# Kernel tuning notes

Measured on AMD Instinct MI355X. Metric: run time of the kernel, lower is better.

## Reference

```python
import jax, jax.numpy as jnp
from jax import lax
import numpy as np

BIN_THR = 0.5
ENDPOINT_THR = 8.0
K_WEIGHT = 60.0
THIN_ITERS = 8  # fixed-iteration Zhang-Suen thinning (stand-in for skimage.skeletonize)


def _bce_with_logits(x, y):
    # elementwise binary_cross_entropy_with_logits, reduction='none'
    return jnp.maximum(x, 0.0) - x * y + jnp.log1p(jnp.exp(-jnp.abs(x)))


def _center_zero_kernel(size):
    k = np.ones((1, 1, size, size), dtype=np.float32)
    k[0, 0, size // 2, size // 2] = 0.0
    return jnp.asarray(k)


def _conv2d(img, kernel, pad):
    # img: [N, 1, H, W], kernel: [1, 1, k, k]
    return lax.conv_general_dilated(img, kernel, (1, 1), [(pad, pad), (pad, pad)])


def _thin_substep(img, sub):
    # img: [N, H, W] of {0,1} float32; one Zhang-Suen sub-iteration (sub is a static int)
    N, H, W = img.shape
    p = jnp.pad(img, ((0, 0), (1, 1), (1, 1)))
    sh = lambda dy, dx: p[:, 1 + dy:1 + dy + H, 1 + dx:1 + dx + W]
    # clockwise neighbors p2..p9: N, NE, E, SE, S, SW, W, NW
    nb = [sh(-1, 0), sh(-1, 1), sh(0, 1), sh(1, 1), sh(1, 0), sh(1, -1), sh(0, -1), sh(-1, -1)]
    Bn = sum(nb)  # neighbor count
    trans = sum(((nb[i] < 0.5) & (nb[(i + 1) % 8] > 0.5)).astype(jnp.int32) for i in range(8))
    c1 = (Bn >= 2.0) & (Bn <= 6.0) & (trans == 1)
    p2, p4, p6, p8 = nb[0], nb[2], nb[4], nb[6]
    if sub == 0:
        c2 = (p2 * p4 * p6 == 0.0) & (p4 * p6 * p8 == 0.0)
    else:
        c2 = (p2 * p4 * p8 == 0.0) & (p2 * p6 * p8 == 0.0)
    delete = (img > 0.5) & c1 & c2
    return jnp.where(delete, 0.0, img)


def _skeletonize(img):
    # img: [N, H, W] binary float32
    def body(i, a):
        a = _thin_substep(a, 0)
        a = _thin_substep(a, 1)
        return a
    return lax.fori_loop(0, THIN_ITERS, body, img)


def setup_inputs() -> dict:
    key = jax.random.key(0)
    kx, ky = jax.random.split(key)
    x = jax.random.normal(kx, (16, 4, 512, 512), dtype=jnp.float32)
    y = jax.random.uniform(ky, (16, 4, 512, 512), dtype=jnp.float32)
    return {"x": x, "y": y}


def reference(x, y):
    Bsz, Np, H, W = x.shape
    loss_map = _bce_with_logits(x, y)  # [B, Np, H, W]
    # binarize: softmax over dim 0, threshold -> {0,1}; detached in original
    s = jax.nn.softmax(x, axis=0)
    A = lax.stop_gradient(jnp.where(s >= BIN_THR, 1.0, 0.0))
    # skeletonize each 2D slice
    skel = _skeletonize(A.reshape(Bsz * Np, H, W))  # [B*Np, H, W]
    # endpoint map: 3x3 ones-with-zero-center conv, threshold at 8
    ep_k = _center_zero_kernel(3)
    c_map = _conv2d(skel[:, None], ep_k, pad=1)  # [B*Np, 1, H, W]
    C = (c_map >= ENDPOINT_THR).astype(jnp.float32)
    # weight map: 9x9 ones-with-zero-center conv * K
    nb_k = _center_zero_kernel(9)
    Wmap = _conv2d(C.reshape(Bsz * Np, 1, H, W), nb_k, pad=4) * K_WEIGHT
    Wmap = Wmap.reshape(Bsz, Np, H, W)
    return jnp.mean(loss_map * Wmap)
```

## Files before the change

kernel.cpp:

```cpp
#include <hip/hip_runtime.h>
#include <cstdint>

#define HH 512
#define WW 512
#define NBATCH 16
#define NPRED 4
#define WPR 8
#define NELEM (NBATCH*NPRED*HH*WW)
#define HALO 21
#define OUTR 64
#define NRTOT (OUTR + 2*HALO)
#define LP (WPR+2)
#define NBLK 512
#define NTHR 256


static __device__ __forceinline__ void fadd(uint64_t a, uint64_t b, uint64_t ci,
                                            uint64_t& s, uint64_t& co) {
    uint64_t x = a ^ b;
    s  = x ^ ci;
    co = (a & b) | (ci & x);
}

static __device__ __forceinline__ void faddio(uint64_t& a, uint64_t b, uint64_t& c) {
    uint64_t x = a ^ b;
    uint64_t s = x ^ c;
    c = (a & b) | (c & x);
    a = s;
}

static __device__ __forceinline__ void sum8(const uint64_t q[8],
                                            uint64_t& b0, uint64_t& b1,
                                            uint64_t& b2, uint64_t& b3) {
    uint64_t s0,c0,s1,c1,s2,c2;
    fadd(q[0],q[1],q[2], s0,c0);
    fadd(q[3],q[4],q[5], s1,c1);
    s2 = q[6] ^ q[7]; c2 = q[6] & q[7];
    uint64_t ca; fadd(s0,s1,s2, b0, ca);
    uint64_t t, cb; fadd(c0,c1,c2, t, cb);
    b1 = t ^ ca; uint64_t cc = t & ca;
    b2 = cb ^ cc; b3 = cb & cc;
}

static __device__ __forceinline__ void acc74(uint64_t w[7], uint64_t b0, uint64_t b1,
                                             uint64_t b2, uint64_t b3) {
    uint64_t c;
    { uint64_t x = w[0] ^ b0; c = w[0] & b0; w[0] = x; }
    faddio(w[1], b1, c);
    faddio(w[2], b2, c);
    faddio(w[3], b3, c);
    { uint64_t x = w[4] ^ c; c = w[4] & c; w[4] = x; }
    { uint64_t x = w[5] ^ c; c = w[5] & c; w[5] = x; }
    w[6] ^= c;
}


__global__ void k_binarize(const float* __restrict__ x, uint64_t* __restrict__ pack) {
    int tid = blockIdx.x * blockDim.x + threadIdx.x;
    int w = tid & (WW-1);
    int h = (tid >> 9) & (HH-1);
    int p = tid >> 18;
    int lane = threadIdx.x & 63;
    float v[NBATCH], e[NBATCH];
    float m = -3.4e38f;
    int base = (p*HH + h)*WW + w;
    #pragma unroll
    for (int b = 0; b < NBATCH; ++b) {
        v[b] = x[(size_t)b*(NPRED*HH*WW) + base];
        m = fmaxf(m, v[b]);
    }
    float S = 0.f;
    #pragma unroll
    for (int b = 0; b < NBATCH; ++b) { e[b] = expf(v[b] - m); S += e[b]; }
    float hS = 0.5f * S;
    unsigned long long mymask = 0ULL;
    #pragma unroll
    for (int b = 0; b < NBATCH; ++b) {
        unsigned long long mk = __ballot(e[b] >= hS);
        if (lane == b) mymask = mk;
    }
    if (lane < NBATCH) {
        int slice = lane * NPRED + p;
        pack[((size_t)slice*HH + h)*WPR + (w >> 6)] = mymask;
    }
}

__global__ __launch_bounds__(NTHR) void k_thin_wmap(const uint64_t* __restrict__ pack,
                                                    const float* __restrict__ x,
                                                    const float* __restrict__ y,
                                                    double* __restrict__ partials) {
    __shared__ uint64_t A[(NRTOT+2)*LP];
    __shared__ uint64_t B[(NRTOT+2)*LP];
    __shared__ uint64_t Hs[4*72*WPR];
    __shared__ int chg[16];
    __shared__ int cflag;
    __shared__ double sdata[NTHR];

    const int s    = blockIdx.x >> 3;
    const int base = (blockIdx.x & 7) << 6;
    const int R0   = base - HALO;
    const int tid  = threadIdx.x;

    for (int i = tid; i < (NRTOT+2)*LP; i += NTHR) { A[i] = 0; B[i] = 0; }
    if (tid < 16) chg[tid] = 0;
    if (tid == 0) cflag = 0;
    __syncthreads();
    for (int i = tid; i < NRTOT*WPR; i += NTHR) {
        int lr = i >> 3, c = i & 7;
        int r = R0 + lr;
        if ((unsigned)r < (unsigned)HH)
            A[(lr+1)*LP + c + 1] = pack[((size_t)s*HH + r)*WPR + c];
    }
    __syncthreads();

    uint64_t* cur = A; uint64_t* nxt = B;
    int stable = 0;
    for (int step = 0; step < 16; ++step) {
        if (stable >= 2) break;
        bool mych = false;
        for (int i = tid; i < NRTOT*WPR; i += NTHR) {
            int lr = i >> 3, c = i & 7;
            int o = (lr+1)*LP + c + 1;
            uint64_t up = cur[o-LP-1], uc = cur[o-LP], un = cur[o-LP+1];
            uint64_t mp = cur[o-1],    mc = cur[o],    mn = cur[o+1];
            uint64_t dp = cur[o+LP-1], dc = cur[o+LP], dn = cur[o+LP+1];
            uint64_t p2 = uc;
            uint64_t p3 = (uc>>1)|(un<<63);
            uint64_t p4 = (mc>>1)|(mn<<63);
            uint64_t p5 = (dc>>1)|(dn<<63);
            uint64_t p6 = dc;
            uint64_t p7 = (dc<<1)|(dp>>63);
            uint64_t p8 = (mc<<1)|(mp>>63);
            uint64_t p9 = (uc<<1)|(up>>63);
            uint64_t qq[8] = {p2,p3,p4,p5,p6,p7,p8,p9};
            uint64_t n0,n1,n2,n3; sum8(qq,n0,n1,n2,n3);
            uint64_t condB = (n1|n2|n3) & ~(n3 | (n2&n1&n0));
            uint64_t tq[8];
            #pragma unroll
            for (int k = 0; k < 8; ++k) tq[k] = ~qq[k] & qq[(k+1)&7];
            uint64_t t0,t1,t2,t3; sum8(tq,t0,t1,t2,t3);
            uint64_t trans1 = t0 & ~(t1|t2|t3);
            uint64_t cond2 = (step & 1) ? (~(p2&p4&p8) & ~(p2&p6&p8))
                                        : (~(p2&p4&p6) & ~(p4&p6&p8));
            uint64_t nv = mc & ~(condB & trans1 & cond2);
            nxt[o] = nv;
            mych |= (nv != mc);
        }
        if (mych) chg[step] = 1;
        __syncthreads();
        stable = chg[step] ? 0 : stable + 1;
        uint64_t* t = cur; cur = nxt; nxt = t;
    }

    uint64_t* Cb = nxt;
    for (int i = tid; i < 72*WPR; i += NTHR) {
        int lr = (i >> 3) + 17, c = i & 7;
        int o = (lr+1)*LP + c + 1;
        uint64_t up = cur[o-LP-1], uc = cur[o-LP], un = cur[o-LP+1];
        uint64_t mp = cur[o-1],    mc = cur[o],    mn = cur[o+1];
        uint64_t dp = cur[o+LP-1], dc = cur[o+LP], dn = cur[o+LP+1];
        uint64_t p3 = (uc>>1)|(un<<63);
        uint64_t p4 = (mc>>1)|(mn<<63);
        uint64_t p5 = (dc>>1)|(dn<<63);
        uint64_t p7 = (dc<<1)|(dp>>63);
        uint64_t p8 = (mc<<1)|(mp>>63);
        uint64_t p9 = (uc<<1)|(up>>63);
        uint64_t cv = uc & p3 & p4 & p5 & dc & p7 & p8 & p9;
        Cb[o] = cv;
        if (cv) cflag = 1;
    }
    __syncthreads();

    if (!cflag) {
        if (tid == 0) partials[blockIdx.x] = 0.0;
        return;
    }

    for (int i = tid; i < 72*WPR; i += NTHR) {
        int hr = i >> 3, c = i & 7;
        int o = (hr+18)*LP + c + 1;
        uint64_t mp = Cb[o-1], mc = Cb[o], mn = Cb[o+1];
        uint64_t m[8];
        m[0] = (mc>>1)|(mn<<63); m[1] = (mc>>2)|(mn<<62);
        m[2] = (mc>>3)|(mn<<61); m[3] = (mc>>4)|(mn<<60);
        m[4] = (mc<<1)|(mp>>63); m[5] = (mc<<2)|(mp>>62);
        m[6] = (mc<<3)|(mp>>61); m[7] = (mc<<4)|(mp>>60);
        uint64_t b0,b1,b2,b3; sum8(m,b0,b1,b2,b3);
        uint64_t inc = mc;
        uint64_t s0 = b0 ^ inc; inc &= b0;
        uint64_t s1 = b1 ^ inc; inc &= b1;
        uint64_t s2 = b2 ^ inc; inc &= b2;
        uint64_t s3 = b3 ^ inc;
        Hs[0*576 + i] = s0; Hs[1*576 + i] = s1;
        Hs[2*576 + i] = s2; Hs[3*576 + i] = s3;
    }
    __syncthreads();

    double acc = 0.0;
    for (int i = tid; i < OUTR*WPR; i += NTHR) {
        int orr = i >> 3, c = i & 7;
        uint64_t w[7];
        int h0 = orr*WPR + c;
        w[0] = Hs[0*576 + h0]; w[1] = Hs[1*576 + h0];
        w[2] = Hs[2*576 + h0]; w[3] = Hs[3*576 + h0];
        w[4] = 0; w[5] = 0; w[6] = 0;
        #pragma unroll
        for (int d = 1; d < 9; ++d) {
            int hh = (orr+d)*WPR + c;
            acc74(w, Hs[0*576+hh], Hs[1*576+hh], Hs[2*576+hh], Hs[3*576+hh]);
        }
        uint64_t cb = Cb[(orr+HALO+1)*LP + c + 1];
        #pragma unroll
        for (int j = 0; j < 7; ++j) {
            uint64_t t = w[j];
            w[j] = t ^ cb;
            cb &= ~t;
        }
        uint64_t any = w[0]|w[1]|w[2]|w[3]|w[4]|w[5]|w[6];
        if (any) {
            size_t pix0 = ((size_t)s*HH + (base + orr))*WW + ((size_t)c << 6);
            uint64_t rem = any;
            while (rem) {
                int bit = __builtin_ctzll(rem);
                rem &= rem - 1;
                int wv = 0;
                #pragma unroll
                for (int j = 0; j < 7; ++j) wv |= (int)((w[j] >> bit) & 1ULL) << j;
                size_t idx = pix0 + bit;
                float lx = x[idx], ly = y[idx];
                float loss = fmaxf(lx, 0.f) - lx*ly + log1pf(expf(-fabsf(lx)));
                acc += (double)(loss * (60.0f * (float)wv));
            }
        }
    }
    sdata[tid] = acc;
    __syncthreads();
    for (int s2 = NTHR/2; s2 > 0; s2 >>= 1) {
        if (tid < s2) sdata[tid] += sdata[tid + s2];
        __syncthreads();
    }
    if (tid == 0) partials[blockIdx.x] = sdata[0];
}

__global__ void k_reduce(const double* __restrict__ partials, float* __restrict__ out,
                         int nparts) {
    __shared__ double sdata[256];
    double a = 0.0;
    for (int i = threadIdx.x; i < nparts; i += 256) a += partials[i];
    sdata[threadIdx.x] = a;
    __syncthreads();
    for (int s2 = 128; s2 > 0; s2 >>= 1) {
        if (threadIdx.x < s2) sdata[threadIdx.x] += sdata[threadIdx.x + s2];
        __syncthreads();
    }
    if (threadIdx.x == 0) out[0] = (float)(sdata[0] / (double)NELEM);
}


extern "C" void kernel_launch(void* const* d_in, const int* in_sizes, int n_in,
                              void* d_out, int out_size, void* d_ws, size_t ws_size,
                              hipStream_t stream) {
    const float* x = (const float*)d_in[0];
    const float* y = (const float*)d_in[1];
    char* ws = (char*)d_ws;
    uint64_t* packA    = (uint64_t*)(ws);
    double*   partials = (double*)  (ws + (2u<<20));

    k_binarize<<<4096, 256, 0, stream>>>(x, packA);
    k_thin_wmap<<<NBLK, NTHR, 0, stream>>>(packA, x, y, partials);
    k_reduce<<<1, 256, 0, stream>>>(partials, (float*)d_out, NBLK);
}
```

Baseline: 31.65 us.

## Vectorize binarize, halve thinning tiles, shrink halo per step, fuse final reduction

Binarize now loads float4 and uses a log-threshold test with fast exp/log, then transposes nibbles through shared memory to build packed words. The thinning kernel uses 32-row tiles over 1024 blocks and narrows the active row range each step as the valid halo shrinks, so rows that cannot affect the output are skipped. The histogram buffer reuses the ping-pong array, and the separate reduce kernel is replaced by a last-block-done atomic counter to save a launch. The price is more halo overhead per tile, a wider LDS row pitch, and a fast-math threshold that could flip borderline pixels.

```diff
diff --git a/kernel.cpp b/kernel.cpp
--- a/kernel.cpp
+++ b/kernel.cpp
@@ -8,11 +8,13 @@
 #define WPR 8
 #define NELEM (NBATCH*NPRED*HH*WW)
 #define HALO 21
-#define OUTR 64
+#define OUTR 32
 #define NRTOT (OUTR + 2*HALO)
-#define LP (WPR+2)
-#define NBLK 512
+#define LP 24
+#define NBLK 1024
 #define NTHR 256
+#define CROWS (OUTR + 8)
+#define HPL (CROWS*WPR)
 
 
 static __device__ __forceinline__ void fadd(uint64_t a, uint64_t b, uint64_t ci,
@@ -55,49 +57,66 @@
 }
 
 
-__global__ void k_binarize(const float* __restrict__ x, uint64_t* __restrict__ pack) {
-    int tid = blockIdx.x * blockDim.x + threadIdx.x;
-    int w = tid & (WW-1);
-    int h = (tid >> 9) & (HH-1);
-    int p = tid >> 18;
-    int lane = threadIdx.x & 63;
-    float v[NBATCH], e[NBATCH];
-    float m = -3.4e38f;
-    int base = (p*HH + h)*WW + w;
+__global__ __launch_bounds__(256) void k_binarize(const float* __restrict__ x,
+                                                  uint64_t* __restrict__ pack,
+                                                  unsigned int* __restrict__ cnt) {
+    if (blockIdx.x == 0 && threadIdx.x == 0) *cnt = 0u;
+    __shared__ uint64_t nibs[272];
+    const int t = blockIdx.x * 256 + threadIdx.x;
+    const float4* __restrict__ xv = reinterpret_cast<const float4*>(x);
+    float4 va[NBATCH];
+    #pragma unroll
+    for (int b = 0; b < NBATCH; ++b) va[b] = xv[(size_t)b * (NPRED*HH*WW/4) + t];
+    float4 mx = va[0];
+    #pragma unroll
+    for (int b = 1; b < NBATCH; ++b) {
+        mx.x = fmaxf(mx.x, va[b].x); mx.y = fmaxf(mx.y, va[b].y);
+        mx.z = fmaxf(mx.z, va[b].z); mx.w = fmaxf(mx.w, va[b].w);
+    }
+    float sx=0.f, sy=0.f, sz=0.f, sw=0.f;
     #pragma unroll
     for (int b = 0; b < NBATCH; ++b) {
-        v[b] = x[(size_t)b*(NPRED*HH*WW) + base];
-        m = fmaxf(m, v[b]);
-    }
-    float S = 0.f;
-    #pragma unroll
-    for (int b = 0; b < NBATCH; ++b) { e[b] = expf(v[b] - m); S += e[b]; }
-    float hS = 0.5f * S;
-    unsigned long long mymask = 0ULL;
+        sx += __expf(va[b].x - mx.x); sy += __expf(va[b].y - mx.y);
+        sz += __expf(va[b].z - mx.z); sw += __expf(va[b].w - mx.w);
+    }
+    const float tx = mx.x + __logf(0.5f*sx), ty = mx.y + __logf(0.5f*sy);
+    const float tz = mx.z + __logf(0.5f*sz), tw = mx.w + __logf(0.5f*sw);
+    uint64_t nib = 0;
     #pragma unroll
     for (int b = 0; b < NBATCH; ++b) {
-        unsigned long long mk = __ballot(e[b] >= hS);
-        if (lane == b) mymask = mk;
-    }
-    if (lane < NBATCH) {
-        int slice = lane * NPRED + p;
-        pack[((size_t)slice*HH + h)*WPR + (w >> 6)] = mymask;
-    }
+        unsigned n = (va[b].x >= tx ? 1u:0u) | (va[b].y >= ty ? 2u:0u)
+                   | (va[b].z >= tz ? 4u:0u) | (va[b].w >= tw ? 8u:0u);
+        nib |= (uint64_t)n << (4*b);
+    }
+    nibs[threadIdx.x + (threadIdx.x >> 4)] = nib;
+    __syncthreads();
+    const int wg = threadIdx.x >> 4, b = threadIdx.x & 15;
+    uint64_t word = 0;
+    #pragma unroll
+    for (int j = 0; j < 16; ++j)
+        word |= ((nibs[wg*17 + j] >> (4*b)) & 0xFULL) << (4*j);
+    const int wgg = blockIdx.x * 16 + wg;
+    const int wword = wgg & 7;
+    const int h = (wgg >> 3) & (HH-1);
+    const int p = wgg >> 12;
+    pack[((size_t)(b*NPRED + p)*HH + h)*WPR + wword] = word;
 }
 
 __global__ __launch_bounds__(NTHR) void k_thin_wmap(const uint64_t* __restrict__ pack,
                                                     const float* __restrict__ x,
                                                     const float* __restrict__ y,
-                                                    double* __restrict__ partials) {
+                                                    double* __restrict__ partials,
+                                                    unsigned int* __restrict__ cnt,
+                                                    float* __restrict__ out) {
     __shared__ uint64_t A[(NRTOT+2)*LP];
     __shared__ uint64_t B[(NRTOT+2)*LP];
-    __shared__ uint64_t Hs[4*72*WPR];
+    __shared__ double sdata[NTHR];
     __shared__ int chg[16];
     __shared__ int cflag;
-    __shared__ double sdata[NTHR];
-
-    const int s    = blockIdx.x >> 3;
-    const int base = (blockIdx.x & 7) << 6;
+    __shared__ int lastFlag;
+
+    const int s    = blockIdx.x >> 4;
+    const int base = (blockIdx.x & 15) << 5;
     const int R0   = base - HALO;
     const int tid  = threadIdx.x;
 
@@ -115,12 +134,14 @@
 
     uint64_t* cur = A; uint64_t* nxt = B;
     int stable = 0;
-    for (int step = 0; step < 16; ++step) {
-        if (stable >= 2) break;
+    for (int step = 0; step < 16 && stable < 2; ++step) {
+        const int lo = step + 1;
+        const int nw = (NRTOT - 2 - 2*step) * WPR;
         bool mych = false;
-        for (int i = tid; i < NRTOT*WPR; i += NTHR) {
-            int lr = i >> 3, c = i & 7;
-            int o = (lr+1)*LP + c + 1;
+        for (int i = tid; i < nw; i += NTHR) {
+            const int lr = (i >> 3) + lo;
+            const int c = i & 7;
+            const int o = (lr+1)*LP + c + 1;
             uint64_t up = cur[o-LP-1], uc = cur[o-LP], un = cur[o-LP+1];
             uint64_t mp = cur[o-1],    mc = cur[o],    mn = cur[o+1];
             uint64_t dp = cur[o+LP-1], dc = cur[o+LP], dn = cur[o+LP+1];
@@ -149,13 +170,14 @@
         if (mych) chg[step] = 1;
         __syncthreads();
         stable = chg[step] ? 0 : stable + 1;
-        uint64_t* t = cur; cur = nxt; nxt = t;
+        uint64_t* tmp = cur; cur = nxt; nxt = tmp;
     }
 
     uint64_t* Cb = nxt;
-    for (int i = tid; i < 72*WPR; i += NTHR) {
-        int lr = (i >> 3) + 17, c = i & 7;
-        int o = (lr+1)*LP + c + 1;
+    for (int i = tid; i < CROWS*WPR; i += NTHR) {
+        const int lr = (i >> 3) + (HALO - 4);
+        const int c = i & 7;
+        const int o = (lr+1)*LP + c + 1;
         uint64_t up = cur[o-LP-1], uc = cur[o-LP], un = cur[o-LP+1];
         uint64_t mp = cur[o-1],    mc = cur[o],    mn = cur[o+1];
         uint64_t dp = cur[o+LP-1], dc = cur[o+LP], dn = cur[o+LP+1];
@@ -171,89 +193,95 @@
     }
     __syncthreads();
 
-    if (!cflag) {
-        if (tid == 0) partials[blockIdx.x] = 0.0;
-        return;
-    }
-
-    for (int i = tid; i < 72*WPR; i += NTHR) {
-        int hr = i >> 3, c = i & 7;
-        int o = (hr+18)*LP + c + 1;
-        uint64_t mp = Cb[o-1], mc = Cb[o], mn = Cb[o+1];
-        uint64_t m[8];
-        m[0] = (mc>>1)|(mn<<63); m[1] = (mc>>2)|(mn<<62);
-        m[2] = (mc>>3)|(mn<<61); m[3] = (mc>>4)|(mn<<60);
-        m[4] = (mc<<1)|(mp>>63); m[5] = (mc<<2)|(mp>>62);
-        m[6] = (mc<<3)|(mp>>61); m[7] = (mc<<4)|(mp>>60);
-        uint64_t b0,b1,b2,b3; sum8(m,b0,b1,b2,b3);
-        uint64_t inc = mc;
-        uint64_t s0 = b0 ^ inc; inc &= b0;
-        uint64_t s1 = b1 ^ inc; inc &= b1;
-        uint64_t s2 = b2 ^ inc; inc &= b2;
-        uint64_t s3 = b3 ^ inc;
-        Hs[0*576 + i] = s0; Hs[1*576 + i] = s1;
-        Hs[2*576 + i] = s2; Hs[3*576 + i] = s3;
-    }
-    __syncthreads();
-
     double acc = 0.0;
-    for (int i = tid; i < OUTR*WPR; i += NTHR) {
-        int orr = i >> 3, c = i & 7;
-        uint64_t w[7];
-        int h0 = orr*WPR + c;
-        w[0] = Hs[0*576 + h0]; w[1] = Hs[1*576 + h0];
-        w[2] = Hs[2*576 + h0]; w[3] = Hs[3*576 + h0];
-        w[4] = 0; w[5] = 0; w[6] = 0;
-        #pragma unroll
-        for (int d = 1; d < 9; ++d) {
-            int hh = (orr+d)*WPR + c;
-            acc74(w, Hs[0*576+hh], Hs[1*576+hh], Hs[2*576+hh], Hs[3*576+hh]);
+    if (cflag) {
+        uint64_t* Hp = cur;
+        for (int i = tid; i < CROWS*WPR; i += NTHR) {
+            const int hr = i >> 3, c = i & 7;
+            const int o = (hr + HALO - 3)*LP + c + 1;
+            uint64_t mp = Cb[o-1], mc = Cb[o], mn = Cb[o+1];
+            uint64_t m[8];
+            m[0] = (mc>>1)|(mn<<63); m[1] = (mc>>2)|(mn<<62);
+            m[2] = (mc>>3)|(mn<<61); m[3] = (mc>>4)|(mn<<60);
+            m[4] = (mc<<1)|(mp>>63); m[5] = (mc<<2)|(mp>>62);
+            m[6] = (mc<<3)|(mp>>61); m[7] = (mc<<4)|(mp>>60);
+            uint64_t b0,b1,b2,b3; sum8(m,b0,b1,b2,b3);
+            uint64_t inc = mc;
+            uint64_t s0 = b0 ^ inc; inc &= b0;
+            uint64_t s1 = b1 ^ inc; inc &= b1;
+            uint64_t s2 = b2 ^ inc; inc &= b2;
+            uint64_t s3 = b3 ^ inc;
+            Hp[0*HPL + i] = s0; Hp[1*HPL + i] = s1;
+            Hp[2*HPL + i] = s2; Hp[3*HPL + i] = s3;
         }
-        uint64_t cb = Cb[(orr+HALO+1)*LP + c + 1];
-        #pragma unroll
-        for (int j = 0; j < 7; ++j) {
-            uint64_t t = w[j];
-            w[j] = t ^ cb;
-            cb &= ~t;
-        }
-        uint64_t any = w[0]|w[1]|w[2]|w[3]|w[4]|w[5]|w[6];
-        if (any) {
-            size_t pix0 = ((size_t)s*HH + (base + orr))*WW + ((size_t)c << 6);
-            uint64_t rem = any;
-            while (rem) {
-                int bit = __builtin_ctzll(rem);
-                rem &= rem - 1;
-                int wv = 0;
-                #pragma unroll
-                for (int j = 0; j < 7; ++j) wv |= (int)((w[j] >> bit) & 1ULL) << j;
-                size_t idx = pix0 + bit;
-                float lx = x[idx], ly = y[idx];
-                float loss = fmaxf(lx, 0.f) - lx*ly + log1pf(expf(-fabsf(lx)));
-                acc += (double)(loss * (60.0f * (float)wv));
+        __syncthreads();
+        {
+            const int i = tid;
+            const int orr = i >> 3, c = i & 7;
+            uint64_t w[7];
+            const int h0 = orr*WPR + c;
+            w[0] = Hp[h0]; w[1] = Hp[HPL + h0]; w[2] = Hp[2*HPL + h0]; w[3] = Hp[3*HPL + h0];
+            w[4] = 0; w[5] = 0; w[6] = 0;
+            #pragma unroll
+            for (int d = 1; d < 9; ++d) {
+                const int hh = (orr+d)*WPR + c;
+                acc74(w, Hp[hh], Hp[HPL+hh], Hp[2*HPL+hh], Hp[3*HPL+hh]);
+            }
+            uint64_t cb = Cb[(orr + HALO + 1)*LP + c + 1];
+            #pragma unroll
+            for (int j = 0; j < 7; ++j) {
+                uint64_t t = w[j];
+                w[j] = t ^ cb;
+                cb &= ~t;
+            }
+            uint64_t any = w[0]|w[1]|w[2]|w[3]|w[4]|w[5]|w[6];
+            if (any) {
+                size_t pix0 = ((size_t)s*HH + (base + orr))*WW + ((size_t)c << 6);
+                uint64_t rem = any;
+                while (rem) {
+                    int bit = __builtin_ctzll(rem);
+                    rem &= rem - 1;
+                    int wv = 0;
+                    #pragma unroll
+                    for (int j = 0; j < 7; ++j) wv |= (int)((w[j] >> bit) & 1ULL) << j;
+                    size_t idx = pix0 + bit;
+                    float lx = x[idx], ly = y[idx];
+                    float loss = fmaxf(lx, 0.f) - lx*ly + log1pf(expf(-fabsf(lx)));
+                    acc += (double)(loss * (60.0f * (float)wv));
+                }
             }
         }
     }
+
     sdata[tid] = acc;
     __syncthreads();
     for (int s2 = NTHR/2; s2 > 0; s2 >>= 1) {
         if (tid < s2) sdata[tid] += sdata[tid + s2];
         __syncthreads();
     }
-    if (tid == 0) partials[blockIdx.x] = sdata[0];
-}
-
-__global__ void k_reduce(const double* __restrict__ partials, float* __restrict__ out,
-                         int nparts) {
-    __shared__ double sdata[256];
+    if (tid == 0) {
+        __hip_atomic_store(&partials[blockIdx.x], sdata[0],
+                           __ATOMIC_RELEASE, __HIP_MEMORY_SCOPE_AGENT);
+        unsigned old = __hip_atomic_fetch_add(cnt, 1u,
+                           __ATOMIC_ACQ_REL, __HIP_MEMORY_SCOPE_AGENT);
+        lastFlag = (old == NBLK - 1);
+    }
+    __syncthreads();
+    if (!lastFlag) return;
+
     double a = 0.0;
-    for (int i = threadIdx.x; i < nparts; i += 256) a += partials[i];
-    sdata[threadIdx.x] = a;
-    __syncthreads();
-    for (int s2 = 128; s2 > 0; s2 >>= 1) {
-        if (threadIdx.x < s2) sdata[threadIdx.x] += sdata[threadIdx.x + s2];
+    for (int i = tid; i < NBLK; i += NTHR)
+        a += __hip_atomic_load(&partials[i], __ATOMIC_RELAXED, __HIP_MEMORY_SCOPE_AGENT);
+    sdata[tid] = a;
+    __syncthreads();
+    for (int s2 = NTHR/2; s2 > 0; s2 >>= 1) {
+        if (tid < s2) sdata[tid] += sdata[tid + s2];
         __syncthreads();
     }
-    if (threadIdx.x == 0) out[0] = (float)(sdata[0] / (double)NELEM);
+    if (tid == 0) {
+        out[0] = (float)(sdata[0] / (double)NELEM);
+        __hip_atomic_store(cnt, 0u, __ATOMIC_RELAXED, __HIP_MEMORY_SCOPE_AGENT);
+    }
 }
 
 
@@ -263,10 +291,10 @@
     const float* x = (const float*)d_in[0];
     const float* y = (const float*)d_in[1];
     char* ws = (char*)d_ws;
-    uint64_t* packA    = (uint64_t*)(ws);
-    double*   partials = (double*)  (ws + (2u<<20));
-
-    k_binarize<<<4096, 256, 0, stream>>>(x, packA);
-    k_thin_wmap<<<NBLK, NTHR, 0, stream>>>(packA, x, y, partials);
-    k_reduce<<<1, 256, 0, stream>>>(partials, (float*)d_out, NBLK);
-}
+    double*       partials = (double*)(ws);
+    unsigned int* cnt      = (unsigned int*)(ws + 8192);
+    uint64_t*     packA    = (uint64_t*)(ws + 16384);
+
+    k_binarize<<<1024, 256, 0, stream>>>(x, packA, cnt);
+    k_thin_wmap<<<NBLK, NTHR, 0, stream>>>(packA, x, y, partials, cnt, (float*)d_out);
+}
```

After: 55.87 us. 1.76x slower.
